# Optimization experiments

Hardware: AMD Instinct MI355X
Metric: run time of the kernel (lower is better)

## Reference

```python
import jax, jax.numpy as jnp
import numpy as np

NUM_NEURONS = 65536
T_STEPS = 1024
V_TH = 1.0
V_RESET = 0.0
TAU = 20.0
DT = 1.0


def setup_inputs() -> dict:
    key = jax.random.key(0)
    input_current = jax.random.normal(key, (T_STEPS, NUM_NEURONS), dtype=jnp.float32)
    return {"input_current": input_current}


def reference(input_current) -> jnp.ndarray:
    """LIF recurrence. The original loops over the batch axis while each
    neuron object carries membrane potential V across rows, so the batch
    axis is sequential (time). Vectorized over neurons, lax.scan over time.

    V <- V + dt/tau * (-(V - V_reset) + I)
    spike = V >= V_th ; V <- V_reset where spiked
    """
    alpha = jnp.float32(DT / TAU)

    def step(V, I):
        V = V + alpha * (V_RESET - V + I)
        spike = V >= V_TH
        V = jnp.where(spike, jnp.float32(V_RESET), V)
        return V, spike.astype(jnp.float32)

    V0 = jnp.full((input_current.shape[1],), V_RESET, dtype=jnp.float32)
    _, spikes = jax.lax.scan(step, V0, input_current)
    return spikes  # (T, N) binary float32
```

## Files before the change

kernel.cpp:

```cpp
#include <hip/hip_runtime.h>


#define T_STEPS 1024
#define NUM_NEURONS 65536
#define N NUM_NEURONS
#define BLOCK 256
#define U 32
#define NCHUNK (T_STEPS / U)

__global__ __launch_bounds__(BLOCK) void lif_kernel(const float* __restrict__ in,
                                                    float* __restrict__ out) {
    __shared__ unsigned int words[NCHUNK][BLOCK];

    const int tid = threadIdx.x;
    const int gid = blockIdx.x * BLOCK + tid;
    constexpr float alpha = 0.05f;
    constexpr float vth = 1.0f;

    const float* __restrict__ p = in + gid;

    float V = 0.0f;
    float I[U], J[U];

#pragma unroll
    for (int u = 0; u < U; ++u) I[u] = p[(size_t)u * N];

    for (int k = 0; k < NCHUNK - 1; ++k) {
#pragma unroll
        for (int u = 0; u < U; ++u) J[u] = p[(size_t)((k + 1) * U + u) * N];

        unsigned int w = 0u;
#pragma unroll
        for (int u = 0; u < U; ++u) {
            V = V + alpha * (I[u] - V);
            const bool s = (V >= vth);
            w |= s ? (1u << u) : 0u;
            V = s ? 0.0f : V;
        }
        words[k][tid] = w;

#pragma unroll
        for (int u = 0; u < U; ++u) I[u] = J[u];
    }

    {
        unsigned int w = 0u;
#pragma unroll
        for (int u = 0; u < U; ++u) {
            V = V + alpha * (I[u] - V);
            const bool s = (V >= vth);
            w |= s ? (1u << u) : 0u;
            V = s ? 0.0f : V;
        }
        words[NCHUNK - 1][tid] = w;
    }

    float* __restrict__ q = out + gid;
    for (int k = 0; k < NCHUNK; ++k) {
        const unsigned int w = words[k][tid];
#pragma unroll
        for (int u = 0; u < U; ++u) {
            const float s = (w & (1u << u)) ? 1.0f : 0.0f;
            __builtin_nontemporal_store(s, q + (size_t)(k * U + u) * N);
        }
    }
}

extern "C" void kernel_launch(void* const* d_in, const int* in_sizes, int n_in,
                              void* d_out, int out_size, void* d_ws, size_t ws_size,
                              hipStream_t stream) {
    const float* in = (const float*)d_in[0];
    float* out = (float*)d_out;
    lif_kernel<<<NUM_NEURONS / BLOCK, BLOCK, 0, stream>>>(in, out);
}
```

Measured before the change: 435.9 us.

## Interleave spike stores with input prefetch instead of buffering all spikes in LDS

```diff
diff --git a/kernel.cpp b/kernel.cpp
--- a/kernel.cpp
+++ b/kernel.cpp
@@ -5,30 +5,28 @@
 #define NUM_NEURONS 65536
 #define N NUM_NEURONS
 #define BLOCK 256
-#define U 32
+#define U 16
 #define NCHUNK (T_STEPS / U)
 
 __global__ __launch_bounds__(BLOCK) void lif_kernel(const float* __restrict__ in,
                                                     float* __restrict__ out) {
-    __shared__ unsigned int words[NCHUNK][BLOCK];
-
-    const int tid = threadIdx.x;
-    const int gid = blockIdx.x * BLOCK + tid;
+    const int gid = blockIdx.x * BLOCK + threadIdx.x;
     constexpr float alpha = 0.05f;
     constexpr float vth = 1.0f;
 
     const float* __restrict__ p = in + gid;
+    float* __restrict__ q = out + gid;
 
     float V = 0.0f;
     float I[U], J[U];
+    unsigned int prevw = 0u;
 
 #pragma unroll
     for (int u = 0; u < U; ++u) I[u] = p[(size_t)u * N];
 
-    for (int k = 0; k < NCHUNK - 1; ++k) {
+    {
 #pragma unroll
-        for (int u = 0; u < U; ++u) J[u] = p[(size_t)((k + 1) * U + u) * N];
-
+        for (int u = 0; u < U; ++u) J[u] = p[(size_t)(U + u) * N];
         unsigned int w = 0u;
 #pragma unroll
         for (int u = 0; u < U; ++u) {
@@ -37,12 +35,37 @@
             w |= s ? (1u << u) : 0u;
             V = s ? 0.0f : V;
         }
-        words[k][tid] = w;
-
+        prevw = w;
 #pragma unroll
         for (int u = 0; u < U; ++u) I[u] = J[u];
     }
 
+    for (int k = 1; k < NCHUNK - 1; ++k) {
+#pragma unroll
+        for (int u = 0; u < U; ++u) J[u] = p[(size_t)((k + 1) * U + u) * N];
+#pragma unroll
+        for (int u = 0; u < U; ++u) {
+            const float s = (prevw & (1u << u)) ? 1.0f : 0.0f;
+            __builtin_nontemporal_store(s, q + (size_t)((k - 1) * U + u) * N);
+        }
+        unsigned int w = 0u;
+#pragma unroll
+        for (int u = 0; u < U; ++u) {
+            V = V + alpha * (I[u] - V);
+            const bool s = (V >= vth);
+            w |= s ? (1u << u) : 0u;
+            V = s ? 0.0f : V;
+        }
+        prevw = w;
+#pragma unroll
+        for (int u = 0; u < U; ++u) I[u] = J[u];
+    }
+
+#pragma unroll
+    for (int u = 0; u < U; ++u) {
+        const float s = (prevw & (1u << u)) ? 1.0f : 0.0f;
+        __builtin_nontemporal_store(s, q + (size_t)((NCHUNK - 2) * U + u) * N);
+    }
     {
         unsigned int w = 0u;
 #pragma unroll
@@ -52,16 +75,10 @@
             w |= s ? (1u << u) : 0u;
             V = s ? 0.0f : V;
         }
-        words[NCHUNK - 1][tid] = w;
-    }
-
-    float* __restrict__ q = out + gid;
-    for (int k = 0; k < NCHUNK; ++k) {
-        const unsigned int w = words[k][tid];
 #pragma unroll
         for (int u = 0; u < U; ++u) {
             const float s = (w & (1u << u)) ? 1.0f : 0.0f;
-            __builtin_nontemporal_store(s, q + (size_t)(k * U + u) * N);
+            __builtin_nontemporal_store(s, q + (size_t)((NCHUNK - 1) * U + u) * N);
         }
     }
 }
```

Result: no change. 437.8 us (+0.4%).
